# Kernel tuning notes

Measured on AMD Instinct MI355X. Metric: run time of the kernel, lower is better.

Reference implementation:

```python
import jax, jax.numpy as jnp
import numpy as np

EPS = 1e-6
B, N, I, H, O, L = 8, 2048, 64, 128, 8, 3
K = O * L
ITERS, TAU, LAM, KNN = 3, 0.1, 0.5, 5

def _ln(x, g, b):
    m = x.mean(-1, keepdims=True)
    v = jnp.mean((x - m) ** 2, -1, keepdims=True)
    return (x - m) / jnp.sqrt(v + 1e-5) * g + b

def _gelu(x):
    return jax.nn.gelu(x, approximate=False)


def setup_inputs():
    ks = jax.random.split(jax.random.key(0), 16)
    rn = lambda k, sh, s=0.05: jax.random.normal(k, sh, jnp.float32) * s
    return {
        'x': jax.random.normal(ks[0], (B, N, I), jnp.float32),
        'enc_w1': rn(ks[1], (H, I)), 'enc_b1': jnp.zeros((H,), jnp.float32),
        'enc_g1': jnp.ones((H,), jnp.float32), 'enc_bb1': jnp.zeros((H,), jnp.float32),
        'enc_w2': rn(ks[2], (H, H)), 'enc_b2': jnp.zeros((H,), jnp.float32),
        'enc_g2': jnp.ones((H,), jnp.float32), 'enc_bb2': jnp.zeros((H,), jnp.float32),
        'sp_w1': rn(ks[3], (H, H + 1)), 'sp_b1': jnp.zeros((H,), jnp.float32),
        'sp_g': jnp.ones((H,), jnp.float32), 'sp_bb': jnp.zeros((H,), jnp.float32),
        'sp_w2': rn(ks[4], (1, H), 0.005), 'sp_b2': jnp.zeros((1,), jnp.float32),
        'object_space': rn(ks[5], (1, O, H), 0.1),
        'horizon_scale': jnp.float32(0.3),
        'level_times': jnp.array([1.0, 2.5, 4.0], jnp.float32),
        'base_horizons': jnp.array([0.9, 0.6, 0.3], jnp.float32),
        'gru_w_ih': rn(ks[6], (3 * H, H)), 'gru_w_hh': rn(ks[7], (3 * H, H)),
        'gru_b_ih': jnp.zeros((3 * H,), jnp.float32), 'gru_b_hh': jnp.zeros((3 * H,), jnp.float32),
        'mlp_w1': rn(ks[8], (H, H)), 'mlp_b1': jnp.zeros((H,), jnp.float32),
        'mlp_w2': rn(ks[9], (H, H)), 'mlp_b2': jnp.zeros((H,), jnp.float32),
        'norm_g': jnp.ones((H,), jnp.float32), 'norm_b': jnp.zeros((H,), jnp.float32),
    }


def reference(x, enc_w1, enc_b1, enc_g1, enc_bb1, enc_w2, enc_b2, enc_g2, enc_bb2, sp_w1, sp_b1, sp_g, sp_bb, sp_w2, sp_b2, object_space, horizon_scale, level_times, base_horizons, gru_w_ih, gru_w_hh, gru_b_ih, gru_b_hh, mlp_w1, mlp_b1, mlp_w2, mlp_b2, norm_g, norm_b):
    # feature encoder: Linear -> LN -> GELU -> Linear -> LN
    h = _gelu(_ln(x @ enc_w1.T + enc_b1, enc_g1, enc_bb1))
    spatial = _ln(h @ enc_w2.T + enc_b2, enc_g2, enc_bb2)  # (B,N,H)
    # local density via kNN mean distance (torch.cdist equivalent)
    sq = jnp.sum(x * x, -1)
    d2 = sq[:, :, None] + sq[:, None, :] - 2.0 * jnp.einsum('bnd,bmd->bnm', x, x)
    dist = jnp.sqrt(jnp.maximum(d2, 0.0))
    knn = -jax.lax.top_k(-dist, KNN + 1)[0]           # k+1 smallest, ascending
    density = jnp.tanh(knn[..., 1:].mean(-1))          # (B,N)
    # scale predictor: Linear -> LN -> GELU -> Linear -> Softplus
    s = jnp.concatenate([spatial, density[..., None]], -1)
    s = _gelu(_ln(s @ sp_w1.T + sp_b1, sp_g, sp_bb))
    pred_scale = jax.nn.softplus(s @ sp_w2.T + sp_b2)  # (B,N,1)
    pred_time = 5.0 - 1.5 * density[..., None] + 0.5 * pred_scale
    features = jnp.concatenate([pred_time, spatial], -1)  # (B,N,H+1)
    # scale-adaptive horizons, tiled object-major to match slot layout
    hz = jnp.clip(base_horizons[None, :, None] + (horizon_scale * (density - 0.5))[:, None, :], 0.1, 1.0)
    horizons = jnp.tile(hz, (1, O, 1))                 # (B,K,N)
    # worldlines
    obj = jnp.broadcast_to(object_space, (B, O, H))
    times = jnp.broadcast_to(jnp.tile(level_times, O)[None, :, None], (B, K, 1))
    slots = jnp.concatenate([times, jnp.repeat(obj, L, axis=1)], -1)  # (B,K,H+1)
    feats_sp = features[..., 1:]
    old_flat = obj.reshape(-1, H)
    attn = None
    for _ in range(ITERS):
        diff = features[:, None, :, :] - slots[:, :, None, :]  # (B,K,N,H+1)
        dt = diff[..., 0]
        dr2 = jnp.sum(diff[..., 1:] ** 2, -1)
        ls = dt * dt - dr2
        d_L = jnp.sign(ls) * jnp.sqrt(jnp.abs(ls) + EPS)
        r = jnp.sqrt(dr2)
        cone = horizons - r / (jnp.abs(dt) + EPS) - 10.0 * jax.nn.relu(-dt) - 5.0 * jax.nn.relu(r - jnp.abs(dt))
        logits = -jnp.abs(d_L) + LAM * jnp.tanh(cone)
        attn = jax.nn.softmax(logits / TAU, axis=1)      # softmax over slots
        w = attn / (attn.sum(2, keepdims=True) + 1e-8)
        upd = jnp.einsum('bkn,bnh->bkh', w, feats_sp)
        obj_upd = upd.reshape(B, O, L, H).sum(2).reshape(-1, H)
        # GRUCell (torch semantics)
        gi = obj_upd @ gru_w_ih.T + gru_b_ih
        gh = old_flat @ gru_w_hh.T + gru_b_hh
        gi_r, gi_z, gi_n = jnp.split(gi, 3, -1)
        gh_r, gh_z, gh_n = jnp.split(gh, 3, -1)
        rg = jax.nn.sigmoid(gi_r + gh_r)
        zg = jax.nn.sigmoid(gi_z + gh_z)
        ng = jnp.tanh(gi_n + rg * gh_n)
        new = ((1.0 - zg) * ng + zg * old_flat).reshape(B, O, H)
        t = _gelu(_ln(new, norm_g, norm_b) @ mlp_w1.T + mlp_b1) @ mlp_w2.T + mlp_b2
        new = new + 0.2 * t
        slots = jnp.concatenate([times, jnp.repeat(new, L, axis=1)], -1)
    return slots, attn, pred_time[..., 0], density
```

## Files before the change

### kernel.cpp

```cpp
#include <hip/hip_runtime.h>
#include <math.h>

constexpr int cB = 8, cN = 2048, cI = 64, cH = 128, cO = 8, cK = 24;
constexpr int ROWS = cB * cN;

constexpr size_t WS_SPATIAL = 0;
constexpr size_t WS_SQ      = WS_SPATIAL + (size_t)ROWS * cH;
constexpr size_t WS_GHS     = WS_SQ + ROWS;
constexpr size_t WS_NSQ0    = WS_GHS + (size_t)cO * 3 * cH;
constexpr size_t WS_NEWOBJ  = WS_NSQ0 + cO;
constexpr size_t WS_NSQ     = WS_NEWOBJ + (size_t)cB * cO * cH;
constexpr size_t WS_WFRAG   = WS_NSQ + (size_t)cB * cO;
constexpr size_t WS_UPD3    = WS_WFRAG + 45056;
constexpr size_t WS_S3      = WS_UPD3 + (size_t)3 * cB * cK * cH;
constexpr size_t WS_XBF     = WS_S3 + (size_t)3 * cB * cK;

constexpr size_t WF_W1H = 0;
constexpr size_t WF_W1L = 8192;
constexpr size_t WF_W2H = 16384;
constexpr size_t WF_W2L = 32768;
constexpr size_t WF_WHH = 49152;
constexpr size_t WF_WHL = 69632;

constexpr size_t OUT_SLOTS = 0;
constexpr size_t OUT_ATTN  = (size_t)cB * cK * 129;
constexpr size_t OUT_PT    = OUT_ATTN + (size_t)cB * cK * cN;
constexpr size_t OUT_DEN   = OUT_PT + (size_t)cB * cN;

typedef __attribute__((ext_vector_type(8))) short bf16x8;
typedef __attribute__((ext_vector_type(4))) float f32x4;

__device__ __forceinline__ float gelu_f(float v){
  return 0.5f * v * (1.f + erff(v * 0.70710678118654752440f));
}
__device__ __forceinline__ short f2bf(float f){
  unsigned u = __float_as_uint(f);
  u += 0x7fffu + ((u >> 16) & 1u);
  return (short)(u >> 16);
}
__device__ __forceinline__ float bf2f(short h){
  return __uint_as_float(((unsigned)(unsigned short)h) << 16);
}
__device__ __forceinline__ bf16x8 pack8(float4 a, float4 b){
  bf16x8 r;
  r[0]=f2bf(a.x); r[1]=f2bf(a.y); r[2]=f2bf(a.z); r[3]=f2bf(a.w);
  r[4]=f2bf(b.x); r[5]=f2bf(b.y); r[6]=f2bf(b.z); r[7]=f2bf(b.w);
  return r;
}
__device__ __forceinline__ float qred16(float a){
  a += __shfl_xor(a, 1); a += __shfl_xor(a, 2); a += __shfl_xor(a, 4); a += __shfl_xor(a, 8);
  return a;
}
__device__ __forceinline__ void load_split_frag(const float* buf, int off, bf16x8& hi, bf16x8& lo){
  float4 u0 = *(const float4*)&buf[off];
  float4 u1 = *(const float4*)&buf[off + 4];
  float v[8] = {u0.x,u0.y,u0.z,u0.w,u1.x,u1.y,u1.z,u1.w};
  #pragma unroll
  for (int i = 0; i < 8; ++i){
    short h = f2bf(v[i]);
    hi[i] = h;
    lo[i] = f2bf(v[i] - bf2f(h));
  }
}
__device__ __forceinline__ int lidx(int row, int col, int stride){
  return row * stride + (col ^ ((row & 3) << 3));
}

__global__ __launch_bounds__(256) void k_cvt_sq(const float* __restrict__ x, short* __restrict__ xbf,
                                                float* __restrict__ sq){
  int t = threadIdx.x;
  size_t base = (size_t)blockIdx.x * 2048;
  int r = t >> 3, e0 = (t & 7) * 8;
  const float4* xp = (const float4*)(x + base + (size_t)r * cI + e0);
  float4 v0 = xp[0], v1 = xp[1];
  *(bf16x8*)(xbf + base + (size_t)r * cI + e0) = pack8(v0, v1);
  float s = v0.x*v0.x + v0.y*v0.y + v0.z*v0.z + v0.w*v0.w
          + v1.x*v1.x + v1.y*v1.y + v1.z*v1.z + v1.w*v1.w;
  s += __shfl_xor(s, 1); s += __shfl_xor(s, 2); s += __shfl_xor(s, 4);
  if ((t & 7) == 0) sq[blockIdx.x * 32 + r] = s;
}

__global__ __launch_bounds__(256) void k_prep(const float* __restrict__ objsp, const float* __restrict__ w_hh,
                                              const float* __restrict__ b_hh,
                                              const float* __restrict__ ew1, const float* __restrict__ ew2,
                                              const float* __restrict__ spw1,
                                              float* __restrict__ ghs, float* __restrict__ nsq0,
                                              short* __restrict__ wf){
  int id = blockIdx.x * 256 + threadIdx.x;
  if (id < cO * 3 * cH){
    int o = id / (3 * cH), j = id % (3 * cH);
    const float* wr = w_hh + (size_t)j * cH;
    const float* ob = objsp + (size_t)o * cH;
    float a0=0,a1=0,a2=0,a3=0;
    #pragma unroll
    for (int h = 0; h < cH; h += 4){
      a0 += wr[h]*ob[h]; a1 += wr[h+1]*ob[h+1]; a2 += wr[h+2]*ob[h+2]; a3 += wr[h+3]*ob[h+3];
    }
    ghs[id] = (a0+a1)+(a2+a3) + b_hh[j];
  } else if (id < cO * 3 * cH + cO){
    int o = id - cO * 3 * cH;
    const float* ob = objsp + (size_t)o * cH;
    float s = 0.f;
    for (int h = 0; h < cH; ++h) s += ob[h]*ob[h];
    nsq0[o] = s;
  } else {
    int idx = id - (cO * 3 * cH + cO);
    if (idx >= 45056) return;
    float w; size_t hoff, loff;
    int e, nc;
    if (idx < 8192){
      e = idx; nc = 2;
      int i = e & 7, l = (e >> 3) & 63, r = e >> 9;
      int c = r % nc, ft = r / nc;
      int f = ft * 16 + (l & 15), k = c * 32 + (l >> 4) * 8 + i;
      w = ew1[f * cI + k];
      hoff = WF_W1H + e; loff = WF_W1L + e;
    } else if (idx < 24576){
      e = idx - 8192; nc = 4;
      int i = e & 7, l = (e >> 3) & 63, r = e >> 9;
      int c = r % nc, ft = r / nc;
      int f = ft * 16 + (l & 15), k = c * 32 + (l >> 4) * 8 + i;
      w = ew2[f * cH + k];
      hoff = WF_W2H + e; loff = WF_W2L + e;
    } else {
      e = idx - 24576; nc = 5;
      int i = e & 7, l = (e >> 3) & 63, r = e >> 9;
      int c = r % nc, ft = r / nc;
      int f = ft * 16 + (l & 15), k = c * 32 + (l >> 4) * 8 + i;
      w = (k < 129) ? spw1[f * 129 + k] : 0.f;
      hoff = WF_WHH + e; loff = WF_WHL + e;
    }
    short h = f2bf(w);
    wf[hoff] = h;
    wf[loff] = f2bf(w - bf2f(h));
  }
}

__global__ __launch_bounds__(256) void k_pairwise(const short* __restrict__ xbf, const float* __restrict__ sq,
                                                  float* __restrict__ den_out){
  __shared__ float cand[4][16][101];
  int b  = blockIdx.x >> 7;
  int rt = blockIdx.x & 127;
  int r0 = rt * 16;
  int lane = threadIdx.x & 63, w = threadIdx.x >> 6;
  const short* xb = xbf + (size_t)b * cN * cI;

  int arow = r0 + (lane & 15);
  int koff = (lane >> 4) * 8;
  const bf16x8* ap = (const bf16x8*)(xb + (size_t)arow * cI + koff);
  bf16x8 a0 = ap[0];
  bf16x8 a1 = ap[4];

  float sqr[4];
  int rg0 = r0 + ((lane >> 4) << 2);
  #pragma unroll
  for (int j = 0; j < 4; ++j) sqr[j] = sq[b * cN + rg0 + j];

  float t6[4][6];
  #pragma unroll
  for (int j = 0; j < 4; ++j){
    #pragma unroll
    for (int q = 0; q < 6; ++q) t6[j][q] = 3e38f;
  }

  int cbase = w * 512;
  #pragma unroll 2
  for (int ct = 0; ct < 32; ++ct){
    int col0 = cbase + ct * 16;
    int brow = col0 + (lane & 15);
    const bf16x8* bp = (const bf16x8*)(xb + (size_t)brow * cI + koff);
    bf16x8 b0 = bp[0];
    bf16x8 b1 = bp[4];
    f32x4 acc = {0.f, 0.f, 0.f, 0.f};
    acc = __builtin_amdgcn_mfma_f32_16x16x32_bf16(a0, b0, acc, 0, 0, 0);
    acc = __builtin_amdgcn_mfma_f32_16x16x32_bf16(a1, b1, acc, 0, 0, 0);
    float sqc = sq[b * cN + col0 + (lane & 15)];
    #pragma unroll
    for (int j = 0; j < 4; ++j){
      float d2 = sqr[j] + sqc - 2.f * acc[j];
      d2 = fmaxf(d2, 0.f);
      if (d2 < t6[j][5]){
        if (d2 < t6[j][4]){ t6[j][5]=t6[j][4];
          if (d2 < t6[j][3]){ t6[j][4]=t6[j][3];
            if (d2 < t6[j][2]){ t6[j][3]=t6[j][2];
              if (d2 < t6[j][1]){ t6[j][2]=t6[j][1];
                if (d2 < t6[j][0]){ t6[j][1]=t6[j][0]; t6[j][0]=d2; } else t6[j][1]=d2;
              } else t6[j][2]=d2;
            } else t6[j][3]=d2;
          } else t6[j][4]=d2;
        } else t6[j][5]=d2;
      }
    }
  }
  int rloc = (lane >> 4) << 2;
  #pragma unroll
  for (int j = 0; j < 4; ++j){
    #pragma unroll
    for (int q = 0; q < 6; ++q) cand[w][rloc + j][(lane & 15) * 6 + q] = t6[j][q];
  }
  __syncthreads();
  int tt = threadIdx.x;
  if (tt < 64){
    int ww = tt >> 4, rr = tt & 15;
    const float* c = cand[ww][rr];
    float m0=3e38f,m1=3e38f,m2=3e38f,m3=3e38f,m4=3e38f,m5=3e38f;
    #pragma unroll
    for (int q = 0; q < 96; ++q){
      float v = c[q];
      if (v < m5){
        if (v<m4){ m5=m4; if (v<m3){ m4=m3; if (v<m2){ m3=m2; if (v<m1){ m2=m1; if (v<m0){ m1=m0; m0=v; } else m1=v; } else m2=v; } else m3=v; } else m4=v; } else m5=v;
      }
    }
    float* cw = cand[ww][rr];
    cw[0]=m0; cw[1]=m1; cw[2]=m2; cw[3]=m3; cw[4]=m4; cw[5]=m5;
  }
  __syncthreads();
  if (tt < 16){
    float m0=3e38f,m1=3e38f,m2=3e38f,m3=3e38f,m4=3e38f,m5=3e38f;
    #pragma unroll
    for (int ww = 0; ww < 4; ++ww){
      const float* c = cand[ww][tt];
      #pragma unroll
      for (int q = 0; q < 6; ++q){
        float v = c[q];
        if (v < m5){
          if (v<m4){ m5=m4; if (v<m3){ m4=m3; if (v<m2){ m3=m2; if (v<m1){ m2=m1; if (v<m0){ m1=m0; m0=v; } else m1=v; } else m2=v; } else m3=v; } else m4=v; } else m5=v;
        }
      }
    }
    float md = (sqrtf(m1)+sqrtf(m2)+sqrtf(m3)+sqrtf(m4)+sqrtf(m5)) * 0.2f;
    den_out[b * cN + r0 + tt] = tanhf(md);
  }
}

__global__ __launch_bounds__(128) void k_enc_head(const float* __restrict__ x, const float* __restrict__ den_in,
    const short* __restrict__ wf,
    const float* __restrict__ b1, const float* __restrict__ g1, const float* __restrict__ bb1,
    const float* __restrict__ b2, const float* __restrict__ g2, const float* __restrict__ bb2,
    const float* __restrict__ hb1, const float* __restrict__ hg, const float* __restrict__ hbb,
    const float* __restrict__ hw2, const float* __restrict__ hb2,
    float* __restrict__ spatial, float* __restrict__ pt_out){
  __shared__ __align__(16) float xs_[2][16 * 68];
  __shared__ __align__(16) float hs_[2][16 * 164];
  const int t = threadIdx.x, lane = t & 63, wv = t >> 6;
  const int row0 = blockIdx.x * 32 + wv * 16;
  float* xbuf = xs_[wv];
  float* hbuf = hs_[wv];
  const int r15 = lane & 15, q = lane >> 4;
  const int qx = (q ^ (r15 & 3)) << 3;

  {
    const float4* xg = (const float4*)(x + (size_t)row0 * cI);
    #pragma unroll
    for (int k = 0; k < 4; ++k){
      int f4 = k * 64 + lane;
      int row = f4 >> 4, c4 = (f4 & 15) * 4;
      float4 v = xg[f4];
      *(float4*)&xbuf[lidx(row, c4, 68)] = v;
    }
  }
  __syncthreads();

  f32x4 acc[8];
  const short* w1h = wf + WF_W1H; const short* w1l = wf + WF_W1L;
  const short* w2h = wf + WF_W2H; const short* w2l = wf + WF_W2L;
  const short* whh = wf + WF_WHH; const short* whl = wf + WF_WHL;

  #pragma unroll
  for (int ft = 0; ft < 8; ++ft) acc[ft] = (f32x4){0.f,0.f,0.f,0.f};
  #pragma unroll
  for (int c = 0; c < 2; ++c){
    bf16x8 ah, al;
    load_split_frag(xbuf, r15 * 68 + c * 32 + qx, ah, al);
    #pragma unroll
    for (int ft = 0; ft < 8; ++ft){
      bf16x8 bh = *(const bf16x8*)&w1h[(size_t)(((ft*2 + c)*64) + lane) * 8];
      bf16x8 bl = *(const bf16x8*)&w1l[(size_t)(((ft*2 + c)*64) + lane) * 8];
      acc[ft] = __builtin_amdgcn_mfma_f32_16x16x32_bf16(al, bh, acc[ft], 0, 0, 0);
      acc[ft] = __builtin_amdgcn_mfma_f32_16x16x32_bf16(ah, bl, acc[ft], 0, 0, 0);
      acc[ft] = __builtin_amdgcn_mfma_f32_16x16x32_bf16(ah, bh, acc[ft], 0, 0, 0);
    }
  }
  {
    float sm0=0,sm1=0,sm2=0,sm3=0, s20=0,s21=0,s22=0,s23=0;
    #pragma unroll
    for (int ft = 0; ft < 8; ++ft){
      float bv = b1[ft*16 + r15];
      float v0 = acc[ft][0]+bv, v1 = acc[ft][1]+bv, v2 = acc[ft][2]+bv, v3 = acc[ft][3]+bv;
      acc[ft][0]=v0; acc[ft][1]=v1; acc[ft][2]=v2; acc[ft][3]=v3;
      sm0+=v0; sm1+=v1; sm2+=v2; sm3+=v3;
      s20+=v0*v0; s21+=v1*v1; s22+=v2*v2; s23+=v3*v3;
    }
    sm0=qred16(sm0); sm1=qred16(sm1); sm2=qred16(sm2); sm3=qred16(sm3);
    s20=qred16(s20); s21=qred16(s21); s22=qred16(s22); s23=qred16(s23);
    float mean[4] = { sm0*(1.f/128.f), sm1*(1.f/128.f), sm2*(1.f/128.f), sm3*(1.f/128.f) };
    float rstd[4] = { rsqrtf(s20*(1.f/128.f)-mean[0]*mean[0]+1e-5f),
                      rsqrtf(s21*(1.f/128.f)-mean[1]*mean[1]+1e-5f),
                      rsqrtf(s22*(1.f/128.f)-mean[2]*mean[2]+1e-5f),
                      rsqrtf(s23*(1.f/128.f)-mean[3]*mean[3]+1e-5f) };
    #pragma unroll
    for (int ft = 0; ft < 8; ++ft){
      float gv = g1[ft*16 + r15], bbv = bb1[ft*16 + r15];
      #pragma unroll
      for (int j = 0; j < 4; ++j){
        float e = gelu_f((acc[ft][j]-mean[j])*rstd[j]*gv + bbv);
        hbuf[lidx(q*4 + j, ft*16 + r15, 164)] = e;
      }
    }
  }
  __syncthreads();

  #pragma unroll
  for (int ft = 0; ft < 8; ++ft) acc[ft] = (f32x4){0.f,0.f,0.f,0.f};
  #pragma unroll
  for (int c = 0; c < 4; ++c){
    bf16x8 ah, al;
    load_split_frag(hbuf, r15 * 164 + c * 32 + qx, ah, al);
    #pragma unroll
    for (int ft = 0; ft < 8; ++ft){
      bf16x8 bh = *(const bf16x8*)&w2h[(size_t)(((ft*4 + c)*64) + lane) * 8];
      bf16x8 bl = *(const bf16x8*)&w2l[(size_t)(((ft*4 + c)*64) + lane) * 8];
      acc[ft] = __builtin_amdgcn_mfma_f32_16x16x32_bf16(al, bh, acc[ft], 0, 0, 0);
      acc[ft] = __builtin_amdgcn_mfma_f32_16x16x32_bf16(ah, bl, acc[ft], 0, 0, 0);
      acc[ft] = __builtin_amdgcn_mfma_f32_16x16x32_bf16(ah, bh, acc[ft], 0, 0, 0);
    }
  }
  __syncthreads();
  {
    float sm0=0,sm1=0,sm2=0,sm3=0, s20=0,s21=0,s22=0,s23=0;
    #pragma unroll
    for (int ft = 0; ft < 8; ++ft){
      float bv = b2[ft*16 + r15];
      float v0 = acc[ft][0]+bv, v1 = acc[ft][1]+bv, v2 = acc[ft][2]+bv, v3 = acc[ft][3]+bv;
      acc[ft][0]=v0; acc[ft][1]=v1; acc[ft][2]=v2; acc[ft][3]=v3;
      sm0+=v0; sm1+=v1; sm2+=v2; sm3+=v3;
      s20+=v0*v0; s21+=v1*v1; s22+=v2*v2; s23+=v3*v3;
    }
    sm0=qred16(sm0); sm1=qred16(sm1); sm2=qred16(sm2); sm3=qred16(sm3);
    s20=qred16(s20); s21=qred16(s21); s22=qred16(s22); s23=qred16(s23);
    float mean[4] = { sm0*(1.f/128.f), sm1*(1.f/128.f), sm2*(1.f/128.f), sm3*(1.f/128.f) };
    float rstd[4] = { rsqrtf(s20*(1.f/128.f)-mean[0]*mean[0]+1e-5f),
                      rsqrtf(s21*(1.f/128.f)-mean[1]*mean[1]+1e-5f),
                      rsqrtf(s22*(1.f/128.f)-mean[2]*mean[2]+1e-5f),
                      rsqrtf(s23*(1.f/128.f)-mean[3]*mean[3]+1e-5f) };
    #pragma unroll
    for (int ft = 0; ft < 8; ++ft){
      float gv = g2[ft*16 + r15], bbv = bb2[ft*16 + r15];
      #pragma unroll
      for (int j = 0; j < 4; ++j){
        float s = (acc[ft][j]-mean[j])*rstd[j]*gv + bbv;
        hbuf[lidx(q*4 + j, ft*16 + r15, 164)] = s;
      }
    }
    #pragma unroll
    for (int i = 0; i < 8; ++i){
      int flat = lane * 8 + i;
      int row = flat >> 5, col = 128 + (flat & 31);
      float v = ((flat & 31) == 0) ? den_in[row0 + row] : 0.f;
      hbuf[lidx(row, col, 164)] = v;
    }
  }
  __syncthreads();

  {
    #pragma unroll
    for (int k = 0; k < 8; ++k){
      int f4 = k * 64 + lane;
      int row = f4 >> 5, c4 = (f4 & 31) * 4;
      float4 v = *(const float4*)&hbuf[lidx(row, c4, 164)];
      *(float4*)(spatial + (size_t)(row0 + row) * cH + c4) = v;
    }
  }

  #pragma unroll
  for (int ft = 0; ft < 8; ++ft) acc[ft] = (f32x4){0.f,0.f,0.f,0.f};
  #pragma unroll
  for (int c = 0; c < 5; ++c){
    bf16x8 ah, al;
    load_split_frag(hbuf, r15 * 164 + c * 32 + qx, ah, al);
    #pragma unroll
    for (int ft = 0; ft < 8; ++ft){
      bf16x8 bh = *(const bf16x8*)&whh[(size_t)(((ft*5 + c)*64) + lane) * 8];
      bf16x8 bl = *(const bf16x8*)&whl[(size_t)(((ft*5 + c)*64) + lane) * 8];
      acc[ft] = __builtin_amdgcn_mfma_f32_16x16x32_bf16(al, bh, acc[ft], 0, 0, 0);
      acc[ft] = __builtin_amdgcn_mfma_f32_16x16x32_bf16(ah, bl, acc[ft], 0, 0, 0);
      acc[ft] = __builtin_amdgcn_mfma_f32_16x16x32_bf16(ah, bh, acc[ft], 0, 0, 0);
    }
  }
  {
    float sm0=0,sm1=0,sm2=0,sm3=0, s20=0,s21=0,s22=0,s23=0;
    #pragma unroll
    for (int ft = 0; ft < 8; ++ft){
      float bv = hb1[ft*16 + r15];
      float v0 = acc[ft][0]+bv, v1 = acc[ft][1]+bv, v2 = acc[ft][2]+bv, v3 = acc[ft][3]+bv;
      acc[ft][0]=v0; acc[ft][1]=v1; acc[ft][2]=v2; acc[ft][3]=v3;
      sm0+=v0; sm1+=v1; sm2+=v2; sm3+=v3;
      s20+=v0*v0; s21+=v1*v1; s22+=v2*v2; s23+=v3*v3;
    }
    sm0=qred16(sm0); sm1=qred16(sm1); sm2=qred16(sm2); sm3=qred16(sm3);
    s20=qred16(s20); s21=qred16(s21); s22=qred16(s22); s23=qred16(s23);
    float mean[4] = { sm0*(1.f/128.f), sm1*(1.f/128.f), sm2*(1.f/128.f), sm3*(1.f/128.f) };
    float rstd[4] = { rsqrtf(s20*(1.f/128.f)-mean[0]*mean[0]+1e-5f),
                      rsqrtf(s21*(1.f/128.f)-mean[1]*mean[1]+1e-5f),
                      rsqrtf(s22*(1.f/128.f)-mean[2]*mean[2]+1e-5f),
                      rsqrtf(s23*(1.f/128.f)-mean[3]*mean[3]+1e-5f) };
    float part0=0, part1=0, part2=0, part3=0;
    #pragma unroll
    for (int ft = 0; ft < 8; ++ft){
      float gv = hg[ft*16 + r15], bbv = hbb[ft*16 + r15], w2v = hw2[ft*16 + r15];
      part0 += gelu_f((acc[ft][0]-mean[0])*rstd[0]*gv + bbv) * w2v;
      part1 += gelu_f((acc[ft][1]-mean[1])*rstd[1]*gv + bbv) * w2v;
      part2 += gelu_f((acc[ft][2]-mean[2])*rstd[2]*gv + bbv) * w2v;
      part3 += gelu_f((acc[ft][3]-mean[3])*rstd[3]*gv + bbv) * w2v;
    }
    part0=qred16(part0); part1=qred16(part1); part2=qred16(part2); part3=qred16(part3);
    float parts[4] = { part0, part1, part2, part3 };
    #pragma unroll
    for (int j = 0; j < 4; ++j){
      if (r15 == j){
        int row = q * 4 + j;
        float ps = parts[j] + hb2[0];
        float spl = fmaxf(ps, 0.f) + log1pf(expf(-fabsf(ps)));
        float dn = den_in[row0 + row];
        pt_out[row0 + row] = 5.f - 1.5f*dn + 0.5f*spl;
      }
    }
  }
}

__global__ __launch_bounds__(256) void k_attn_upd(const float* __restrict__ spatial, const float* __restrict__ pt_in,
    const float* __restrict__ den_in, const float* __restrict__ objp, int ob_stride,
    const float* __restrict__ nsqp, int nq_stride,
    const float* __restrict__ lt, const float* __restrict__ bh, const float* __restrict__ hs,
    float* __restrict__ attn_out, int writeAttn,
    float* __restrict__ upd_raw, float* __restrict__ Ssum){
  __shared__ float abuf[24][65];
  int blk = blockIdx.x;
  int b = blk >> 5, chunk = blk & 31;
  int n0 = chunk * 64;
  int t = threadIdx.x;
  int sub = t & 3, rl = t >> 2;
  int id = b * cN + n0 + rl;

  {
    float4 sv[8];
    const float4* sp4 = (const float4*)(spatial + (size_t)id * cH + sub * 32);
    #pragma unroll
    for (int i = 0; i < 8; ++i) sv[i] = sp4[i];
    float spn2 = 0.f;
    #pragma unroll
    for (int i = 0; i < 8; ++i) spn2 += sv[i].x*sv[i].x + sv[i].y*sv[i].y + sv[i].z*sv[i].z + sv[i].w*sv[i].w;

    const float* ob = objp + (size_t)b * ob_stride;
    float acc[8];
    #pragma unroll
    for (int o = 0; o < 8; ++o){
      const float4* orow = (const float4*)(ob + (size_t)o * cH + sub * 32);
      float a0=0,a1=0,a2=0,a3=0;
      #pragma unroll
      for (int i = 0; i < 8; ++i){ float4 w4 = orow[i];
        a0 += w4.x*sv[i].x; a1 += w4.y*sv[i].y; a2 += w4.z*sv[i].z; a3 += w4.w*sv[i].w; }
      acc[o] = (a0+a1)+(a2+a3);
    }
    spn2 += __shfl_xor(spn2, 1); spn2 += __shfl_xor(spn2, 2);
    #pragma unroll
    for (int o = 0; o < 8; ++o){ acc[o] += __shfl_xor(acc[o], 1); acc[o] += __shfl_xor(acc[o], 2); }

    if (sub == 0){
      const float* nq = nsqp + (size_t)b * nq_stride;
      float nsqv_[8];
      #pragma unroll
      for (int o = 0; o < 8; ++o) nsqv_[o] = nq[o];
      float pt = pt_in[id], den = den_in[id];
      float hsv = hs[0];
      float lts[3] = { lt[0], lt[1], lt[2] };
      float bhs[3] = { bh[0], bh[1], bh[2] };

      float logits[24];
      #pragma unroll
      for (int k = 0; k < 24; ++k){
        const int o = k / 3, l = k % 3;
        float dtv = pt - lts[l];
        float dr2 = fmaxf(spn2 + nsqv_[o] - 2.f * acc[o], 0.f);
        float ls  = dtv*dtv - dr2;
        float adL = sqrtf(fabsf(ls) + 1e-6f);
        float r   = sqrtf(dr2);
        float adt = fabsf(dtv);
        float hz  = fminf(fmaxf(bhs[l] + hsv * (den - 0.5f), 0.1f), 1.0f);
        float cone = hz - r / (adt + 1e-6f) - 10.f * fmaxf(-dtv, 0.f) - 5.f * fmaxf(r - adt, 0.f);
        logits[k] = (-adL + 0.5f * tanhf(cone)) * 10.f;
      }
      float mx = -3e38f;
      #pragma unroll
      for (int k = 0; k < 24; ++k) mx = fmaxf(mx, logits[k]);
      float es[24]; float ssum = 0.f;
      #pragma unroll
      for (int k = 0; k < 24; ++k){ es[k] = expf(logits[k] - mx); ssum += es[k]; }
      float inv = 1.f / ssum;
      #pragma unroll
      for (int k = 0; k < 24; ++k) abuf[k][rl] = es[k] * inv;
    }
  }
  __syncthreads();

  if (writeAttn){
    float* ao = attn_out + (size_t)b * cK * cN + n0;
    #pragma unroll
    for (int i = 0; i < 6; ++i){
      int idx = t + i * 256;
      ao[(size_t)(idx >> 6) * cN + (idx & 63)] = abuf[idx >> 6][idx & 63];
    }
  }

  int h = t & 127, g = t >> 7;
  float acc2[12];
  #pragma unroll
  for (int kk = 0; kk < 12; ++kk) acc2[kk] = 0.f;
  const float* sp = spatial + ((size_t)b * cN + n0) * cH + h;
  for (int ni = 0; ni < 64; ++ni){
    float spv = sp[(size_t)ni * cH];
    #pragma unroll
    for (int kk = 0; kk < 12; ++kk) acc2[kk] += abuf[g*12+kk][ni] * spv;
  }
  #pragma unroll
  for (int kk = 0; kk < 12; ++kk)
    atomicAdd(&upd_raw[((size_t)b * cK + g*12+kk) * cH + h], acc2[kk]);
  if (t < 24){
    float s = 0.f;
    #pragma unroll
    for (int j = 0; j < 64; ++j) s += abuf[t][j];
    atomicAdd(&Ssum[b * cK + t], s);
  }
}

__global__ __launch_bounds__(128) void k_gru(const float* __restrict__ upd_raw, const float* __restrict__ Ssum,
    const float* __restrict__ ghs, const float* __restrict__ objsp,
    const float* __restrict__ w_ih, const float* __restrict__ b_ih,
    const float* __restrict__ mw1, const float* __restrict__ mb1,
    const float* __restrict__ mw2, const float* __restrict__ mb2,
    const float* __restrict__ ng_, const float* __restrict__ nb_,
    const float* __restrict__ lt,
    float* __restrict__ newobj, float* __restrict__ nsq,
    float* __restrict__ slots_out, int writeSlots){
  __shared__ float ubuf[cH], lbuf[cH], gbuf[cH], red[8];
  int bo = blockIdx.x; int b = bo >> 3, o = bo & 7;
  int t = threadIdx.x;
  int lane = t & 63, wid = t >> 6;

  float u = 0.f;
  #pragma unroll
  for (int l = 0; l < 3; ++l){
    int k = o * 3 + l;
    float s = Ssum[b * cK + k] + 1e-8f;
    u += upd_raw[((size_t)b * cK + k) * cH + t] / s;
  }
  ubuf[t] = u;
  __syncthreads();

  float gi[3];
  #pragma unroll
  for (int j3 = 0; j3 < 3; ++j3){
    const float* wr = w_ih + ((size_t)j3 * cH + t) * cH;
    float a0=0,a1=0,a2=0,a3=0;
    #pragma unroll
    for (int d = 0; d < cH; d += 4){
      a0 += wr[d]*ubuf[d]; a1 += wr[d+1]*ubuf[d+1]; a2 += wr[d+2]*ubuf[d+2]; a3 += wr[d+3]*ubuf[d+3];
    }
    gi[j3] = (a0+a1)+(a2+a3) + b_ih[j3 * cH + t];
  }
  const float* gh = ghs + (size_t)o * 3 * cH;
  float ghr = gh[t], ghz = gh[cH + t], ghn = gh[2 * cH + t];
  float oldv = objsp[(size_t)o * cH + t];
  float rg = 1.f / (1.f + expf(-(gi[0] + ghr)));
  float zg = 1.f / (1.f + expf(-(gi[1] + ghz)));
  float ngv = tanhf(gi[2] + rg * ghn);
  float nv = (1.f - zg) * ngv + zg * oldv;

  float s1 = nv, s2 = nv * nv;
  #pragma unroll
  for (int m = 1; m < 64; m <<= 1){ s1 += __shfl_xor(s1, m); s2 += __shfl_xor(s2, m); }
  if (lane == 0){ red[wid] = s1; red[4 + wid] = s2; }
  __syncthreads();
  float mean = (red[0] + red[1]) * (1.f/128.f);
  float var  = (red[4] + red[5]) * (1.f/128.f) - mean * mean;
  float ln = (nv - mean) * rsqrtf(var + 1e-5f) * ng_[t] + nb_[t];
  lbuf[t] = ln;
  __syncthreads();

  const float* w1r = mw1 + (size_t)t * cH;
  {
    float a0=0,a1=0,a2=0,a3=0;
    #pragma unroll
    for (int d = 0; d < cH; d += 4){
      a0 += w1r[d]*lbuf[d]; a1 += w1r[d+1]*lbuf[d+1]; a2 += w1r[d+2]*lbuf[d+2]; a3 += w1r[d+3]*lbuf[d+3];
    }
    gbuf[t] = gelu_f((a0+a1)+(a2+a3) + mb1[t]);
  }
  __syncthreads();
  const float* w2r = mw2 + (size_t)t * cH;
  float m2v;
  {
    float a0=0,a1=0,a2=0,a3=0;
    #pragma unroll
    for (int d = 0; d < cH; d += 4){
      a0 += w2r[d]*gbuf[d]; a1 += w2r[d+1]*gbuf[d+1]; a2 += w2r[d+2]*gbuf[d+2]; a3 += w2r[d+3]*gbuf[d+3];
    }
    m2v = (a0+a1)+(a2+a3) + mb2[t];
  }
  float outv = nv + 0.2f * m2v;
  newobj[((size_t)b * cO + o) * cH + t] = outv;

  float qv = outv * outv;
  #pragma unroll
  for (int m = 1; m < 64; m <<= 1) qv += __shfl_xor(qv, m);
  __syncthreads();
  if (lane == 0) red[wid] = qv;
  __syncthreads();
  if (t == 0) nsq[b * cO + o] = red[0] + red[1];

  if (writeSlots){
    #pragma unroll
    for (int l = 0; l < 3; ++l){
      size_t base = ((size_t)b * cK + o * 3 + l) * 129;
      slots_out[base + 1 + t] = outv;
      if (t == 0) slots_out[base] = lt[l];
    }
  }
}

extern "C" void kernel_launch(void* const* d_in, const int* in_sizes, int n_in,
                              void* d_out, int out_size, void* d_ws, size_t ws_size,
                              hipStream_t stream){
  const float* x       = (const float*)d_in[0];
  const float* enc_w1  = (const float*)d_in[1];
  const float* enc_b1  = (const float*)d_in[2];
  const float* enc_g1  = (const float*)d_in[3];
  const float* enc_bb1 = (const float*)d_in[4];
  const float* enc_w2  = (const float*)d_in[5];
  const float* enc_b2  = (const float*)d_in[6];
  const float* enc_g2  = (const float*)d_in[7];
  const float* enc_bb2 = (const float*)d_in[8];
  const float* sp_w1   = (const float*)d_in[9];
  const float* sp_b1   = (const float*)d_in[10];
  const float* sp_g    = (const float*)d_in[11];
  const float* sp_bb   = (const float*)d_in[12];
  const float* sp_w2   = (const float*)d_in[13];
  const float* sp_b2   = (const float*)d_in[14];
  const float* objsp   = (const float*)d_in[15];
  const float* hscale  = (const float*)d_in[16];
  const float* ltimes  = (const float*)d_in[17];
  const float* bhor    = (const float*)d_in[18];
  const float* gw_ih   = (const float*)d_in[19];
  const float* gw_hh   = (const float*)d_in[20];
  const float* gb_ih   = (const float*)d_in[21];
  const float* gb_hh   = (const float*)d_in[22];
  const float* mw1     = (const float*)d_in[23];
  const float* mb1     = (const float*)d_in[24];
  const float* mw2     = (const float*)d_in[25];
  const float* mb2     = (const float*)d_in[26];
  const float* normg   = (const float*)d_in[27];
  const float* normb   = (const float*)d_in[28];
  (void)in_sizes; (void)n_in; (void)out_size; (void)ws_size;

  float* out = (float*)d_out;
  float* ws  = (float*)d_ws;

  float* spatial = ws + WS_SPATIAL;
  float* sq      = ws + WS_SQ;
  float* ghs     = ws + WS_GHS;
  float* nsq0    = ws + WS_NSQ0;
  float* newobj  = ws + WS_NEWOBJ;
  float* nsqv    = ws + WS_NSQ;
  short* wf      = (short*)(ws + WS_WFRAG);
  float* updr3   = ws + WS_UPD3;
  float* Ss3     = ws + WS_S3;
  short* xbf     = (short*)(ws + WS_XBF);

  hipMemsetAsync((void*)updr3, 0, (size_t)(3 * cB * cK * cH + 3 * cB * cK) * sizeof(float), stream);

  k_cvt_sq<<<dim3(ROWS / 32), dim3(256), 0, stream>>>(x, xbf, sq);
  k_prep<<<dim3(189), dim3(256), 0, stream>>>(objsp, gw_hh, gb_hh, enc_w1, enc_w2, sp_w1,
                                              ghs, nsq0, wf);
  k_pairwise<<<dim3(cB * (cN / 16)), dim3(256), 0, stream>>>(xbf, sq, out + OUT_DEN);
  k_enc_head<<<dim3(ROWS / 32), dim3(128), 0, stream>>>(x, out + OUT_DEN, wf,
      enc_b1, enc_g1, enc_bb1, enc_b2, enc_g2, enc_bb2,
      sp_b1, sp_g, sp_bb, sp_w2, sp_b2,
      spatial, out + OUT_PT);

  for (int it = 0; it < 3; ++it){
    float* updr = updr3 + (size_t)it * cB * cK * cH;
    float* Ss   = Ss3 + (size_t)it * cB * cK;
    const float* objp = (it == 0) ? objsp : newobj;
    int obst = (it == 0) ? 0 : cO * cH;
    const float* nqp = (it == 0) ? nsq0 : nsqv;
    int nqst = (it == 0) ? 0 : cO;
    k_attn_upd<<<dim3(cB * 32), dim3(256), 0, stream>>>(spatial, out + OUT_PT, out + OUT_DEN,
                                                        objp, obst, nqp, nqst,
                                                        ltimes, bhor, hscale,
                                                        out + OUT_ATTN, (it == 2) ? 1 : 0,
                                                        updr, Ss);
    k_gru<<<dim3(cB * cO), dim3(128), 0, stream>>>(updr, Ss, ghs, objsp, gw_ih, gb_ih,
                                                   mw1, mb1, mw2, mb2, normg, normb, ltimes,
                                                   newobj, nsqv, out + OUT_SLOTS, (it == 2) ? 1 : 0);
  }
}
```

Baseline: 315.0 us.

## Use branchless med3 top-6 insertion and halve attention chunk size for more blocks

Replaces the nested-branch sorted insertion used for kNN top-6 tracking with a branchless min/med3 network, removing wave divergence in the pairwise distance kernel. Separately, the attention/update kernel now handles 32 points per block with 8 threads per point instead of 64 points with 4 threads. That doubles the grid to 512 blocks for better occupancy on the many CUs. The cost is twice as many atomicAdds into the update and sum buffers, plus an extra shuffle stage per reduction.

```diff
diff --git a/kernel.cpp b/kernel.cpp
--- a/kernel.cpp
+++ b/kernel.cpp
@@ -50,6 +50,15 @@
 __device__ __forceinline__ float qred16(float a){
   a += __shfl_xor(a, 1); a += __shfl_xor(a, 2); a += __shfl_xor(a, 4); a += __shfl_xor(a, 8);
   return a;
+}
+#define INS6(T0,T1,T2,T3,T4,T5,X) { \
+  float _o0=T0,_o1=T1,_o2=T2,_o3=T3,_o4=T4,_o5=T5; \
+  T0 = fminf(_o0, X); \
+  T1 = __builtin_amdgcn_fmed3f(_o0,_o1,X); \
+  T2 = __builtin_amdgcn_fmed3f(_o1,_o2,X); \
+  T3 = __builtin_amdgcn_fmed3f(_o2,_o3,X); \
+  T4 = __builtin_amdgcn_fmed3f(_o3,_o4,X); \
+  T5 = __builtin_amdgcn_fmed3f(_o4,_o5,X); \
 }
 __device__ __forceinline__ void load_split_frag(const float* buf, int off, bf16x8& hi, bf16x8& lo){
   float4 u0 = *(const float4*)&buf[off];
@@ -179,17 +188,7 @@
     for (int j = 0; j < 4; ++j){
       float d2 = sqr[j] + sqc - 2.f * acc[j];
       d2 = fmaxf(d2, 0.f);
-      if (d2 < t6[j][5]){
-        if (d2 < t6[j][4]){ t6[j][5]=t6[j][4];
-          if (d2 < t6[j][3]){ t6[j][4]=t6[j][3];
-            if (d2 < t6[j][2]){ t6[j][3]=t6[j][2];
-              if (d2 < t6[j][1]){ t6[j][2]=t6[j][1];
-                if (d2 < t6[j][0]){ t6[j][1]=t6[j][0]; t6[j][0]=d2; } else t6[j][1]=d2;
-              } else t6[j][2]=d2;
-            } else t6[j][3]=d2;
-          } else t6[j][4]=d2;
-        } else t6[j][5]=d2;
-      }
+      INS6(t6[j][0], t6[j][1], t6[j][2], t6[j][3], t6[j][4], t6[j][5], d2);
     }
   }
   int rloc = (lane >> 4) << 2;
@@ -207,9 +206,7 @@
     #pragma unroll
     for (int q = 0; q < 96; ++q){
       float v = c[q];
-      if (v < m5){
-        if (v<m4){ m5=m4; if (v<m3){ m4=m3; if (v<m2){ m3=m2; if (v<m1){ m2=m1; if (v<m0){ m1=m0; m0=v; } else m1=v; } else m2=v; } else m3=v; } else m4=v; } else m5=v;
-      }
+      INS6(m0, m1, m2, m3, m4, m5, v);
     }
     float* cw = cand[ww][rr];
     cw[0]=m0; cw[1]=m1; cw[2]=m2; cw[3]=m3; cw[4]=m4; cw[5]=m5;
@@ -223,9 +220,7 @@
       #pragma unroll
       for (int q = 0; q < 6; ++q){
         float v = c[q];
-        if (v < m5){
-          if (v<m4){ m5=m4; if (v<m3){ m4=m3; if (v<m2){ m3=m2; if (v<m1){ m2=m1; if (v<m0){ m1=m0; m0=v; } else m1=v; } else m2=v; } else m3=v; } else m4=v; } else m5=v;
-        }
+        INS6(m0, m1, m2, m3, m4, m5, v);
       }
     }
     float md = (sqrtf(m1)+sqrtf(m2)+sqrtf(m3)+sqrtf(m4)+sqrtf(m5)) * 0.2f;
@@ -434,37 +429,39 @@
     const float* __restrict__ lt, const float* __restrict__ bh, const float* __restrict__ hs,
     float* __restrict__ attn_out, int writeAttn,
     float* __restrict__ upd_raw, float* __restrict__ Ssum){
-  __shared__ float abuf[24][65];
+  __shared__ float abuf[24][33];
   int blk = blockIdx.x;
-  int b = blk >> 5, chunk = blk & 31;
-  int n0 = chunk * 64;
+  int b = blk >> 6, chunk = blk & 63;
+  int n0 = chunk * 32;
   int t = threadIdx.x;
-  int sub = t & 3, rl = t >> 2;
+  int sub = t & 7, rl = t >> 3;
   int id = b * cN + n0 + rl;
 
   {
-    float4 sv[8];
-    const float4* sp4 = (const float4*)(spatial + (size_t)id * cH + sub * 32);
-    #pragma unroll
-    for (int i = 0; i < 8; ++i) sv[i] = sp4[i];
+    float4 sv[4];
+    const float4* sp4 = (const float4*)(spatial + (size_t)id * cH + sub * 16);
+    #pragma unroll
+    for (int i = 0; i < 4; ++i) sv[i] = sp4[i];
     float spn2 = 0.f;
     #pragma unroll
-    for (int i = 0; i < 8; ++i) spn2 += sv[i].x*sv[i].x + sv[i].y*sv[i].y + sv[i].z*sv[i].z + sv[i].w*sv[i].w;
+    for (int i = 0; i < 4; ++i) spn2 += sv[i].x*sv[i].x + sv[i].y*sv[i].y + sv[i].z*sv[i].z + sv[i].w*sv[i].w;
 
     const float* ob = objp + (size_t)b * ob_stride;
     float acc[8];
     #pragma unroll
     for (int o = 0; o < 8; ++o){
-      const float4* orow = (const float4*)(ob + (size_t)o * cH + sub * 32);
+      const float4* orow = (const float4*)(ob + (size_t)o * cH + sub * 16);
       float a0=0,a1=0,a2=0,a3=0;
       #pragma unroll
-      for (int i = 0; i < 8; ++i){ float4 w4 = orow[i];
+      for (int i = 0; i < 4; ++i){ float4 w4 = orow[i];
         a0 += w4.x*sv[i].x; a1 += w4.y*sv[i].y; a2 += w4.z*sv[i].z; a3 += w4.w*sv[i].w; }
       acc[o] = (a0+a1)+(a2+a3);
     }
-    spn2 += __shfl_xor(spn2, 1); spn2 += __shfl_xor(spn2, 2);
-    #pragma unroll
-    for (int o = 0; o < 8; ++o){ acc[o] += __shfl_xor(acc[o], 1); acc[o] += __shfl_xor(acc[o], 2); }
+    spn2 += __shfl_xor(spn2, 1); spn2 += __shfl_xor(spn2, 2); spn2 += __shfl_xor(spn2, 4);
+    #pragma unroll
+    for (int o = 0; o < 8; ++o){
+      acc[o] += __shfl_xor(acc[o], 1); acc[o] += __shfl_xor(acc[o], 2); acc[o] += __shfl_xor(acc[o], 4);
+    }
 
     if (sub == 0){
       const float* nq = nsqp + (size_t)b * nq_stride;
@@ -506,9 +503,9 @@
   if (writeAttn){
     float* ao = attn_out + (size_t)b * cK * cN + n0;
     #pragma unroll
-    for (int i = 0; i < 6; ++i){
+    for (int i = 0; i < 3; ++i){
       int idx = t + i * 256;
-      ao[(size_t)(idx >> 6) * cN + (idx & 63)] = abuf[idx >> 6][idx & 63];
+      ao[(size_t)(idx >> 5) * cN + (idx & 31)] = abuf[idx >> 5][idx & 31];
     }
   }
 
@@ -517,7 +514,7 @@
   #pragma unroll
   for (int kk = 0; kk < 12; ++kk) acc2[kk] = 0.f;
   const float* sp = spatial + ((size_t)b * cN + n0) * cH + h;
-  for (int ni = 0; ni < 64; ++ni){
+  for (int ni = 0; ni < 32; ++ni){
     float spv = sp[(size_t)ni * cH];
     #pragma unroll
     for (int kk = 0; kk < 12; ++kk) acc2[kk] += abuf[g*12+kk][ni] * spv;
@@ -528,7 +525,7 @@
   if (t < 24){
     float s = 0.f;
     #pragma unroll
-    for (int j = 0; j < 64; ++j) s += abuf[t][j];
+    for (int j = 0; j < 32; ++j) s += abuf[t][j];
     atomicAdd(&Ssum[b * cK + t], s);
   }
 }
@@ -694,7 +691,7 @@
     int obst = (it == 0) ? 0 : cO * cH;
     const float* nqp = (it == 0) ? nsq0 : nsqv;
     int nqst = (it == 0) ? 0 : cO;
-    k_attn_upd<<<dim3(cB * 32), dim3(256), 0, stream>>>(spatial, out + OUT_PT, out + OUT_DEN,
+    k_attn_upd<<<dim3(cB * 64), dim3(256), 0, stream>>>(spatial, out + OUT_PT, out + OUT_DEN,
                                                         objp, obst, nqp, nqst,
                                                         ltimes, bhor, hscale,
                                                         out + OUT_ATTN, (it == 2) ? 1 : 0,
```

Result: faster. 303.3 us (-3.7%).
